# Kernel optimization log

Measured on AMD Instinct MI355X. Metric: run time of the kernel, lower is better.

Reference implementation:

```python
import jax, jax.numpy as jnp
import numpy as np

B, T, E, H = 4, 2048, 1024, 16
S = E // H

def setup_inputs() -> dict:
    key = jax.random.key(0)
    ks = jax.random.split(key, 4)
    x = jax.random.normal(ks[0], (B, T, E), dtype=jnp.float32)
    Wk = jax.random.normal(ks[1], (E, E), dtype=jnp.float32) * (E ** -0.5)
    Wq = jax.random.normal(ks[2], (E, E), dtype=jnp.float32) * (E ** -0.5)
    Wo = jax.random.normal(ks[3], (E, E), dtype=jnp.float32) * (E ** -0.5)
    bo = jnp.zeros((E,), dtype=jnp.float32)
    return {"x": x, "Wk": Wk, "Wq": Wq, "Wo": Wo, "bo": bo}

def reference(x, Wk, Wq, Wo, bo):
    b, t, e = x.shape
    h, s = H, E // H
    scale = e ** (-0.25)  # original scales q and k each by e**(1/4)
    k = (x @ Wk).reshape(b, t, h, s).transpose(0, 2, 1, 3)  # bhts
    q = (x @ Wq).reshape(b, t, h, s).transpose(0, 2, 1, 3)
    # FAITHFUL to source: values use the KEYS projection (bug in original)
    v = (x @ Wk).reshape(b, t, h, s).transpose(0, 2, 1, 3)
    dot = jnp.einsum('bhqd,bhkd->bhqk', q * scale, k * scale)
    attn = jax.nn.softmax(dot, axis=-1)
    out = jnp.einsum('bhqk,bhkd->bhqd', attn, v)
    out = out.transpose(0, 2, 1, 3).reshape(b, t, e)
    return out @ Wo + bo
```

## Files before the change

### kernel.cpp

```cpp
#include <hip/hip_runtime.h>
#include <hip/hip_bf16.h>
#include <stdint.h>

static constexpr int kB = 4;
static constexpr int kT = 2048;
static constexpr int kE = 1024;
static constexpr int kH = 16;
static constexpr int kS = 64;
static constexpr int kRows = kB * kT;

typedef __attribute__((ext_vector_type(4)))  float    f32x4;
typedef __attribute__((ext_vector_type(16))) float    f32x16;
typedef __attribute__((ext_vector_type(4)))  float    float4v;
typedef __attribute__((ext_vector_type(8)))  __bf16   bf16x8;
typedef __attribute__((ext_vector_type(8)))  short    short8v;
typedef __attribute__((ext_vector_type(4)))  short    short4v;
typedef __attribute__((ext_vector_type(2)))  unsigned u32x2;
typedef __attribute__((ext_vector_type(4)))  unsigned u32x4;

typedef const __attribute__((address_space(1))) void gvoid_t;
typedef __attribute__((address_space(3))) void lvoid_t;

__device__ __forceinline__ short f2bf(float f) {
  union { float f; unsigned u; } c; c.f = f;
  unsigned r = (c.u + 0x7FFFu + ((c.u >> 16) & 1u)) >> 16;
  return (short)(r & 0xFFFFu);
}

__device__ __forceinline__ short bfc(float f) {
  union { __bf16 b; short s; } u; u.b = (__bf16)f; return u.s;
}

__device__ __forceinline__ unsigned cvt_pk(float lo, float hi) {
  unsigned r;
  asm("v_cvt_pk_bf16_f32 %0, %1, %2" : "=v"(r) : "v"(lo), "v"(hi));
  return r;
}

__device__ __forceinline__ void plane_swap(unsigned& a, unsigned& b) {
  asm("v_permlane32_swap_b32 %0, %1" : "+v"(a), "+v"(b));
}

#if __has_builtin(__builtin_amdgcn_exp2f)
__device__ __forceinline__ float fexp2(float x) { return __builtin_amdgcn_exp2f(x); }
#else
__device__ __forceinline__ float fexp2(float x) { return exp2f(x); }
#endif

__global__ __launch_bounds__(256)
void prep(const float* __restrict__ x, const float* __restrict__ Wk,
          const float* __restrict__ Wq, const float* __restrict__ Wo,
          short* __restrict__ Xb, short* __restrict__ WkqT,
          short* __restrict__ WoT) {
  const int bid = blockIdx.x;
  if (bid < 8192) {
    size_t i = ((size_t)bid * 256 + threadIdx.x) * 4;
    float4v v = *(const float4v*)(x + i);
    short4v o;
    o[0] = f2bf(v[0]); o[1] = f2bf(v[1]); o[2] = f2bf(v[2]); o[3] = f2bf(v[3]);
    *(short4v*)(Xb + i) = o;
    return;
  }
  __shared__ float tile[32][33];
  const int tb = bid - 8192;
  const int which = tb >> 10, t = tb & 1023;
  const float* W = (which == 0) ? Wk : ((which == 1) ? Wq : Wo);
  short* WT = (which == 0) ? WkqT : ((which == 1) ? (WkqT + kE * kE) : WoT);
  const int tx = threadIdx.x & 31, ty = threadIdx.x >> 5;
  const int c = (t & 31) * 32, r = (t >> 5) * 32;
  #pragma unroll
  for (int i = ty; i < 32; i += 8)
    tile[i][tx] = W[(size_t)(r + i) * kE + c + tx];
  __syncthreads();
  #pragma unroll
  for (int i = ty; i < 32; i += 8)
    WT[(size_t)(c + i) * kE + r + tx] = f2bf(tile[tx][i]);
}

__global__ __launch_bounds__(256)
void gemm_kq(const short* __restrict__ A, const short* __restrict__ BT,
             short* __restrict__ Kb, short* __restrict__ Qb,
             short* __restrict__ KT, float qs) {
  __shared__ short SMp[16384];
  short* As = SMp;
  short* Bs = SMp + 8192;
  const int tid = threadIdx.x;
  const int w = tid >> 6, lane = tid & 63;
  const int g = lane >> 4, lr = lane & 15;
  const int bid = blockIdx.x;
  const int id = (bid & 7) * 128 + (bid >> 3);
  const int n0 = (id & 15) * 128, m0 = (id >> 4) * 128;
  const int wr = w >> 1, wc = w & 1;
  const int srow = lane >> 3, sch = lane & 7;
  const int swz = lr & 7;

  f32x4 acc[4][4];
  #pragma unroll
  for (int m = 0; m < 4; ++m)
    #pragma unroll
    for (int n = 0; n < 4; ++n)
      #pragma unroll
      for (int r = 0; r < 4; ++r) acc[m][n][r] = 0.f;

  for (int kt = 0; kt < kE; kt += 64) {
    #pragma unroll
    for (int i = 0; i < 4; ++i) {
      const int slot = w * 4 + i;
      const int row = slot * 8 + srow;
      const int sc = sch ^ srow;
      __builtin_amdgcn_global_load_lds(
          (gvoid_t*)(A + (size_t)(m0 + row) * kE + kt + 8 * sc),
          (lvoid_t*)(As + slot * 512), 16, 0, 0);
      __builtin_amdgcn_global_load_lds(
          (gvoid_t*)(BT + (size_t)(n0 + row) * kE + kt + 8 * sc),
          (lvoid_t*)(Bs + slot * 512), 16, 0, 0);
    }
    __syncthreads();
    #pragma unroll
    for (int kk = 0; kk < 2; ++kk) {
      bf16x8 af[4], bfr[4];
      #pragma unroll
      for (int m = 0; m < 4; ++m)
        af[m] = *(const bf16x8*)(As + (wr * 64 + m * 16 + lr) * 64 + (((4 * kk + g) ^ swz) << 3));
      #pragma unroll
      for (int n = 0; n < 4; ++n)
        bfr[n] = *(const bf16x8*)(Bs + (wc * 64 + n * 16 + lr) * 64 + (((4 * kk + g) ^ swz) << 3));
      __builtin_amdgcn_s_setprio(1);
      #pragma unroll
      for (int m = 0; m < 4; ++m)
        #pragma unroll
        for (int n = 0; n < 4; ++n)
          acc[m][n] = __builtin_amdgcn_mfma_f32_16x16x32_bf16(af[m], bfr[n], acc[m][n], 0, 0, 0);
      __builtin_amdgcn_s_setprio(0);
    }
    __syncthreads();
  }

  short* C = (n0 < 1024) ? Kb : Qb;
  const float scale = (n0 < 1024) ? 1.0f : qs;
  const int crow = m0 + wr * 64, ccol = (n0 & 1023) + wc * 64;
  #pragma unroll
  for (int m = 0; m < 4; ++m)
    #pragma unroll
    for (int n = 0; n < 4; ++n)
      #pragma unroll
      for (int r = 0; r < 4; ++r)
        C[(size_t)(crow + m * 16 + 4 * g + r) * kE + ccol + n * 16 + lr] =
            bfc(acc[m][n][r] * scale);

  if (n0 < 1024) {
    const int b = m0 >> 11;
    const int tloc = m0 & 2047;
    short* Lt = SMp;
    #pragma unroll
    for (int half = 0; half < 2; ++half) {
      __syncthreads();
      if (wc == half) {
        #pragma unroll
        for (int m = 0; m < 4; ++m)
          #pragma unroll
          for (int n = 0; n < 4; ++n) {
            u32x2 e;
            e[0] = cvt_pk(acc[m][n][0], acc[m][n][1]);
            e[1] = cvt_pk(acc[m][n][2], acc[m][n][3]);
            *(u32x2*)(Lt + (n * 16 + lr) * 136 + wr * 64 + m * 16 + 4 * g) = e;
          }
      }
      __syncthreads();
      const int sc = tid >> 2;
      const int h = (n0 >> 6) + half;
      short* ktrow = KT + ((size_t)(b * 16 + h) * 64 + sc) * kT + tloc;
      #pragma unroll
      for (int i = 0; i < 4; ++i) {
        const int t4 = (tid & 3) * 32 + i * 8;
        u32x4 v = *(const u32x4*)(Lt + sc * 136 + t4);
        *(u32x4*)(ktrow + t4) = v;
      }
    }
  }
}

__global__ __launch_bounds__(256)
void gemm_bt(const short* __restrict__ A, const short* __restrict__ BT,
             float* __restrict__ C, const float* __restrict__ bias,
             int M, int N, int K) {
  __shared__ short As[128 * 64];
  __shared__ short Bs[128 * 64];
  const int tid = threadIdx.x;
  const int w = tid >> 6, lane = tid & 63;
  const int g = lane >> 4, lr = lane & 15;
  const int bid = blockIdx.x;
  const int id = (bid & 7) * 64 + (bid >> 3);
  const int n0 = (id & 7) * 128, m0 = (id >> 3) * 128;
  const int wr = w >> 1, wc = w & 1;
  const int srow = lane >> 3, sch = lane & 7;
  const int swz = lr & 7;

  f32x4 acc[4][4];
  #pragma unroll
  for (int m = 0; m < 4; ++m)
    #pragma unroll
    for (int n = 0; n < 4; ++n)
      #pragma unroll
      for (int r = 0; r < 4; ++r) acc[m][n][r] = 0.f;

  for (int kt = 0; kt < K; kt += 64) {
    #pragma unroll
    for (int i = 0; i < 4; ++i) {
      const int slot = w * 4 + i;
      const int row = slot * 8 + srow;
      const int sc = sch ^ srow;
      __builtin_amdgcn_global_load_lds(
          (gvoid_t*)(A + (size_t)(m0 + row) * K + kt + 8 * sc),
          (lvoid_t*)(As + slot * 512), 16, 0, 0);
      __builtin_amdgcn_global_load_lds(
          (gvoid_t*)(BT + (size_t)(n0 + row) * K + kt + 8 * sc),
          (lvoid_t*)(Bs + slot * 512), 16, 0, 0);
    }
    __syncthreads();
    #pragma unroll
    for (int kk = 0; kk < 2; ++kk) {
      bf16x8 af[4], bfr[4];
      #pragma unroll
      for (int m = 0; m < 4; ++m)
        af[m] = *(const bf16x8*)(As + (wr * 64 + m * 16 + lr) * 64 + (((4 * kk + g) ^ swz) << 3));
      #pragma unroll
      for (int n = 0; n < 4; ++n)
        bfr[n] = *(const bf16x8*)(Bs + (wc * 64 + n * 16 + lr) * 64 + (((4 * kk + g) ^ swz) << 3));
      __builtin_amdgcn_s_setprio(1);
      #pragma unroll
      for (int m = 0; m < 4; ++m)
        #pragma unroll
        for (int n = 0; n < 4; ++n)
          acc[m][n] = __builtin_amdgcn_mfma_f32_16x16x32_bf16(af[m], bfr[n], acc[m][n], 0, 0, 0);
      __builtin_amdgcn_s_setprio(0);
    }
    __syncthreads();
  }

  const int crow = m0 + wr * 64, ccol = n0 + wc * 64;
  float bv[4];
  #pragma unroll
  for (int n = 0; n < 4; ++n) bv[n] = bias[ccol + n * 16 + lr];
  #pragma unroll
  for (int m = 0; m < 4; ++m)
    #pragma unroll
    for (int n = 0; n < 4; ++n)
      #pragma unroll
      for (int r = 0; r < 4; ++r)
        C[(size_t)(crow + m * 16 + 4 * g + r) * N + ccol + n * 16 + lr] =
            acc[m][n][r] + bv[n];
}

__global__ __launch_bounds__(256, 4)
void attn_kernel(const short* Qb, const short* __restrict__ Kb,
                 const short* __restrict__ KT, short* AO) {
  __shared__ short SM[16384];

  const int tid = threadIdx.x;
  const int w = tid >> 6, lane = tid & 63;
  const int l31 = lane & 31, hi = lane >> 5;
  const int swz = l31 & 7;
  const int bid = blockIdx.x;
  const int id = (bid & 7) * 128 + (bid >> 3);
  const int q0 = (id & 15) * 128;
  const int bh = id >> 4;
  const size_t base = (size_t)(bh >> 4) * kT * kE + (size_t)(bh & 15) * kS;
  const short* Kbh = Kb + base;
  const short* KTbh = KT + (size_t)bh * 64 * kT;

  const int srow_lo = lane >> 3, sch = lane & 7;

  #pragma unroll
  for (int i = 0; i < 2; ++i) {
    const int slot = w * 2 + i, row = slot * 8 + srow_lo;
    const int sc = sch ^ (row & 7);
    __builtin_amdgcn_global_load_lds(
        (gvoid_t*)(Kbh + (size_t)row * kE + 8 * sc),
        (lvoid_t*)(SM + slot * 512), 16, 0, 0);
    __builtin_amdgcn_global_load_lds(
        (gvoid_t*)(KTbh + (size_t)row * kT + 8 * sc),
        (lvoid_t*)(SM + 8192 + slot * 512), 16, 0, 0);
  }

  bf16x8 qB[4];
  #pragma unroll
  for (int ks = 0; ks < 4; ++ks)
    qB[ks] = *(const bf16x8*)(Qb + base +
        (size_t)(q0 + w * 32 + l31) * kE + ks * 16 + hi * 8);

  f32x16 oacc[2];
  #pragma unroll
  for (int r = 0; r < 16; ++r) { oacc[0][r] = 0.f; oacc[1][r] = 0.f; }
  float lsum = 0.f;

  for (int t = 0; t < 32; ++t) {
    __syncthreads();

    if (t < 31) {
      const short* kbt = Kbh + (size_t)(t + 1) * 64 * kE;
      const short* vtt = KTbh + (size_t)(t + 1) * 64;
      short* KtN = SM + ((t + 1) & 1) * 4096;
      short* VtN = SM + 8192 + ((t + 1) & 1) * 4096;
      #pragma unroll
      for (int i = 0; i < 2; ++i) {
        const int slot = w * 2 + i, row = slot * 8 + srow_lo;
        const int sc = sch ^ (row & 7);
        __builtin_amdgcn_global_load_lds(
            (gvoid_t*)(kbt + (size_t)row * kE + 8 * sc),
            (lvoid_t*)(KtN + slot * 512), 16, 0, 0);
        __builtin_amdgcn_global_load_lds(
            (gvoid_t*)(vtt + (size_t)row * kT + 8 * sc),
            (lvoid_t*)(VtN + slot * 512), 16, 0, 0);
      }
    }

    const short* KtC = SM + (t & 1) * 4096;
    const short* VtC = SM + 8192 + (t & 1) * 4096;

    f32x16 sacc[2];
    #pragma unroll
    for (int r = 0; r < 16; ++r) { sacc[0][r] = 0.f; sacc[1][r] = 0.f; }
    #pragma unroll
    for (int ks = 0; ks < 4; ++ks) {
      const int pc = ((2 * ks + hi) ^ swz) << 3;
      bf16x8 kf0 = *(const bf16x8*)(KtC + (l31)      * 64 + pc);
      bf16x8 kf1 = *(const bf16x8*)(KtC + (32 + l31) * 64 + pc);
      __builtin_amdgcn_s_setprio(1);
      sacc[0] = __builtin_amdgcn_mfma_f32_32x32x16_bf16(kf0, qB[ks], sacc[0], 0, 0, 0);
      sacc[1] = __builtin_amdgcn_mfma_f32_32x32x16_bf16(kf1, qB[ks], sacc[1], 0, 0, 0);
      __builtin_amdgcn_s_setprio(0);
    }

    union { unsigned u[4]; bf16x8 v; } pf[4];
    #pragma unroll
    for (int kvf = 0; kvf < 2; ++kvf) {
      float pe[16];
      #pragma unroll
      for (int r = 0; r < 16; ++r) {
        pe[r] = fexp2(sacc[kvf][r]);
        lsum += pe[r];
      }
      #pragma unroll
      for (int sub = 0; sub < 2; ++sub) {
        unsigned a0 = cvt_pk(pe[8 * sub + 0], pe[8 * sub + 1]);
        unsigned b0 = cvt_pk(pe[8 * sub + 4], pe[8 * sub + 5]);
        plane_swap(a0, b0);
        unsigned a1 = cvt_pk(pe[8 * sub + 2], pe[8 * sub + 3]);
        unsigned b1 = cvt_pk(pe[8 * sub + 6], pe[8 * sub + 7]);
        plane_swap(a1, b1);
        pf[2 * kvf + sub].u[0] = a0;
        pf[2 * kvf + sub].u[1] = a1;
        pf[2 * kvf + sub].u[2] = b0;
        pf[2 * kvf + sub].u[3] = b1;
      }
    }

    #pragma unroll
    for (int ks = 0; ks < 4; ++ks) {
      const int pc = ((2 * ks + hi) ^ swz) << 3;
      bf16x8 vf0 = *(const bf16x8*)(VtC + (l31)      * 64 + pc);
      bf16x8 vf1 = *(const bf16x8*)(VtC + (32 + l31) * 64 + pc);
      __builtin_amdgcn_s_setprio(1);
      oacc[0] = __builtin_amdgcn_mfma_f32_32x32x16_bf16(vf0, pf[ks].v, oacc[0], 0, 0, 0);
      oacc[1] = __builtin_amdgcn_mfma_f32_32x32x16_bf16(vf1, pf[ks].v, oacc[1], 0, 0, 0);
      __builtin_amdgcn_s_setprio(0);
    }
  }

  __syncthreads();

  const float ltot = lsum + __shfl_xor(lsum, 32);
  const float inv = 1.f / ltot;
  short* OtW = SM + w * 2176;
  #pragma unroll
  for (int sf = 0; sf < 2; ++sf)
    #pragma unroll
    for (int c = 0; c < 4; ++c) {
      u32x2 e;
      e[0] = cvt_pk(oacc[sf][4 * c + 0] * inv, oacc[sf][4 * c + 1] * inv);
      e[1] = cvt_pk(oacc[sf][4 * c + 2] * inv, oacc[sf][4 * c + 3] * inv);
      *(u32x2*)(OtW + l31 * 68 + sf * 32 + 8 * c + 4 * hi) = e;
    }
  __builtin_amdgcn_s_barrier();
  #pragma unroll
  for (int i = 0; i < 8; ++i) {
    const int row = i * 4 + (lane >> 4);
    u32x2 v = *(const u32x2*)(OtW + row * 68 + (lane & 15) * 4);
    *(u32x2*)(AO + base + (size_t)(q0 + w * 32 + row) * kE + (lane & 15) * 4) = v;
  }
}

extern "C" void kernel_launch(void* const* d_in, const int* in_sizes, int n_in,
                              void* d_out, int out_size, void* d_ws, size_t ws_size,
                              hipStream_t stream) {
  const float* x  = (const float*)d_in[0];
  const float* Wk = (const float*)d_in[1];
  const float* Wq = (const float*)d_in[2];
  const float* Wo = (const float*)d_in[3];
  const float* bo = (const float*)d_in[4];
  float* out = (float*)d_out;

  const size_t nXE = (size_t)kRows * kE;
  const size_t nW  = (size_t)kE * kE;

  short* Xb   = (short*)d_ws;
  short* Kb   = Xb   + nXE;
  short* Qb   = Kb   + nXE;
  short* WkqT = Qb   + nXE;
  short* WoT  = WkqT + 2 * nW;
  short* KTb  = (short*)d_out;
  short* AO   = Qb;

  prep<<<dim3(8192 + 3 * 1024), 256, 0, stream>>>(
      x, Wk, Wq, Wo, Xb, WkqT, WoT);

  gemm_kq<<<dim3(1024), 256, 0, stream>>>(
      Xb, WkqT, Kb, Qb, KTb, 0.03125f * 1.44269504f);

  attn_kernel<<<dim3(1024), 256, 0, stream>>>(Qb, Kb, KTb, AO);

  gemm_bt<<<dim3(512), 256, 0, stream>>>(
      AO, WoT, out, bo, kRows, kE, kE);
}
```

Baseline: 172.5 us.

## Rewrite K/Q projection GEMM as 256x256 double-buffered 8-wave pipelined kernel

Replaces the 128x128, 4-wave K/Q projection GEMM with a 256x256 tile kernel using 8 waves. It double-buffers LDS and interleaves global-to-LDS loads of the next K-slab with MFMA phases, using explicit barriers, waitcnt and priority hints. The larger tile raises reuse per loaded byte, and the overlap is meant to hide load latency. The transposed K write now goes straight from registers to global memory instead of through an LDS staging pass, which may give less coalesced stores. The kernel uses 128KB of LDS and many accumulator registers, which limits occupancy to one block per CU.

```diff
diff --git a/kernel.cpp b/kernel.cpp
--- a/kernel.cpp
+++ b/kernel.cpp
@@ -77,106 +77,192 @@
     WT[(size_t)(c + i) * kE + r + tx] = f2bf(tile[tx][i]);
 }
 
-__global__ __launch_bounds__(256)
-void gemm_kq(const short* __restrict__ A, const short* __restrict__ BT,
-             short* __restrict__ Kb, short* __restrict__ Qb,
-             short* __restrict__ KT, float qs) {
-  __shared__ short SMp[16384];
-  short* As = SMp;
-  short* Bs = SMp + 8192;
+
+__device__ __forceinline__ void kq_stageA(
+    const short* __restrict__ gA, short* nA, int wid, int sl, int sc7) {
+  #pragma unroll
+  for (int h = 0; h < 2; ++h)
+    #pragma unroll
+    for (int i = 0; i < 2; ++i) {
+      const int slot = wid * 2 + i;
+      const int row = slot * 8 + sl;
+      const int sc = sc7 ^ (row & 7);
+      __builtin_amdgcn_global_load_lds(
+          (gvoid_t*)(gA + (size_t)(h * 128 + row) * kE + 8 * sc),
+          (lvoid_t*)(nA + h * 8192 + slot * 512), 16, 0, 0);
+    }
+}
+
+__device__ __forceinline__ void kq_tile(
+    const short* __restrict__ gA, const short* __restrict__ gB,
+    const short* cA, const short* cB, short* nA, short* nB,
+    bool stage, f32x4 (&acc)[8][4],
+    int wid, int wm, int wn, int g, int lr, int sl, int sc7) {
+  const int swz = lr & 7;
+  const short* cAw = cA + wm * 8192;
+  const short* cBw = cB + (wn >> 1) * 8192;
+  const int brow0 = (wn & 1) * 64;
+  bf16x8 af[4][2], b0[2][2], b1[2][2];
+
+  #pragma unroll
+  for (int mf = 0; mf < 4; ++mf)
+    #pragma unroll
+    for (int kk = 0; kk < 2; ++kk)
+      af[mf][kk] = *(const bf16x8*)(cAw + (mf * 16 + lr) * 64 + (((4 * kk + g) ^ swz) << 3));
+  #pragma unroll
+  for (int nf = 0; nf < 2; ++nf)
+    #pragma unroll
+    for (int kk = 0; kk < 2; ++kk)
+      b0[nf][kk] = *(const bf16x8*)(cBw + (brow0 + nf * 16 + lr) * 64 + (((4 * kk + g) ^ swz) << 3));
+  if (stage) kq_stageA(gA, nA, wid, sl, sc7);
+  asm volatile("" ::: "memory");
+  __builtin_amdgcn_s_barrier();
+  asm volatile("s_waitcnt lgkmcnt(0)" ::: "memory");
+  __builtin_amdgcn_sched_barrier(0);
+  __builtin_amdgcn_s_setprio(1);
+  #pragma unroll
+  for (int mf = 0; mf < 4; ++mf)
+    #pragma unroll
+    for (int nf = 0; nf < 2; ++nf)
+      #pragma unroll
+      for (int kk = 0; kk < 2; ++kk)
+        acc[mf][nf] = __builtin_amdgcn_mfma_f32_16x16x32_bf16(af[mf][kk], b0[nf][kk], acc[mf][nf], 0, 0, 0);
+  __builtin_amdgcn_s_setprio(0);
+  asm volatile("" ::: "memory");
+  __builtin_amdgcn_s_barrier();
+
+  #pragma unroll
+  for (int nf = 0; nf < 2; ++nf)
+    #pragma unroll
+    for (int kk = 0; kk < 2; ++kk)
+      b1[nf][kk] = *(const bf16x8*)(cBw + (brow0 + 32 + nf * 16 + lr) * 64 + (((4 * kk + g) ^ swz) << 3));
+  if (stage) kq_stageA(gB, nB, wid, sl, sc7);
+  asm volatile("" ::: "memory");
+  __builtin_amdgcn_s_barrier();
+  asm volatile("s_waitcnt lgkmcnt(0)" ::: "memory");
+  __builtin_amdgcn_sched_barrier(0);
+  __builtin_amdgcn_s_setprio(1);
+  #pragma unroll
+  for (int mf = 0; mf < 4; ++mf)
+    #pragma unroll
+    for (int nf = 0; nf < 2; ++nf)
+      #pragma unroll
+      for (int kk = 0; kk < 2; ++kk)
+        acc[mf][2 + nf] = __builtin_amdgcn_mfma_f32_16x16x32_bf16(af[mf][kk], b1[nf][kk], acc[mf][2 + nf], 0, 0, 0);
+  __builtin_amdgcn_s_setprio(0);
+  asm volatile("" ::: "memory");
+  __builtin_amdgcn_s_barrier();
+
+  #pragma unroll
+  for (int mf = 0; mf < 4; ++mf)
+    #pragma unroll
+    for (int kk = 0; kk < 2; ++kk)
+      af[mf][kk] = *(const bf16x8*)(cAw + (64 + mf * 16 + lr) * 64 + (((4 * kk + g) ^ swz) << 3));
+  asm volatile("" ::: "memory");
+  __builtin_amdgcn_s_barrier();
+  asm volatile("s_waitcnt lgkmcnt(0)" ::: "memory");
+  __builtin_amdgcn_sched_barrier(0);
+  __builtin_amdgcn_s_setprio(1);
+  #pragma unroll
+  for (int mf = 0; mf < 4; ++mf)
+    #pragma unroll
+    for (int nf = 0; nf < 2; ++nf)
+      #pragma unroll
+      for (int kk = 0; kk < 2; ++kk)
+        acc[4 + mf][2 + nf] = __builtin_amdgcn_mfma_f32_16x16x32_bf16(af[mf][kk], b1[nf][kk], acc[4 + mf][2 + nf], 0, 0, 0);
+  __builtin_amdgcn_s_setprio(0);
+  asm volatile("" ::: "memory");
+  __builtin_amdgcn_s_barrier();
+
+  #pragma unroll
+  for (int nf = 0; nf < 2; ++nf)
+    #pragma unroll
+    for (int kk = 0; kk < 2; ++kk)
+      b0[nf][kk] = *(const bf16x8*)(cBw + (brow0 + nf * 16 + lr) * 64 + (((4 * kk + g) ^ swz) << 3));
+  asm volatile("s_waitcnt vmcnt(0)" ::: "memory");
+  asm volatile("" ::: "memory");
+  __builtin_amdgcn_s_barrier();
+  asm volatile("s_waitcnt lgkmcnt(0)" ::: "memory");
+  __builtin_amdgcn_sched_barrier(0);
+  __builtin_amdgcn_s_setprio(1);
+  #pragma unroll
+  for (int mf = 0; mf < 4; ++mf)
+    #pragma unroll
+    for (int nf = 0; nf < 2; ++nf)
+      #pragma unroll
+      for (int kk = 0; kk < 2; ++kk)
+        acc[4 + mf][nf] = __builtin_amdgcn_mfma_f32_16x16x32_bf16(af[mf][kk], b0[nf][kk], acc[4 + mf][nf], 0, 0, 0);
+  __builtin_amdgcn_s_setprio(0);
+  asm volatile("" ::: "memory");
+  __builtin_amdgcn_s_barrier();
+}
+
+__global__ __launch_bounds__(512)
+void gemm_kq8(const short* __restrict__ A, const short* __restrict__ BT,
+              short* __restrict__ Kb, short* __restrict__ Qb,
+              short* __restrict__ KT, float qs) {
+  __shared__ short LA[2][16384];
+  __shared__ short LB[2][16384];
+
   const int tid = threadIdx.x;
-  const int w = tid >> 6, lane = tid & 63;
+  const int wid = tid >> 6, lane = tid & 63;
   const int g = lane >> 4, lr = lane & 15;
+  const int wm = wid >> 2, wn = wid & 3;
+  const int sl = lane >> 3, sc7 = lane & 7;
   const int bid = blockIdx.x;
-  const int id = (bid & 7) * 128 + (bid >> 3);
-  const int n0 = (id & 15) * 128, m0 = (id >> 4) * 128;
-  const int wr = w >> 1, wc = w & 1;
-  const int srow = lane >> 3, sch = lane & 7;
-  const int swz = lr & 7;
-
-  f32x4 acc[4][4];
-  #pragma unroll
-  for (int m = 0; m < 4; ++m)
-    #pragma unroll
-    for (int n = 0; n < 4; ++n)
-      #pragma unroll
-      for (int r = 0; r < 4; ++r) acc[m][n][r] = 0.f;
-
-  for (int kt = 0; kt < kE; kt += 64) {
-    #pragma unroll
-    for (int i = 0; i < 4; ++i) {
-      const int slot = w * 4 + i;
-      const int row = slot * 8 + srow;
-      const int sc = sch ^ srow;
-      __builtin_amdgcn_global_load_lds(
-          (gvoid_t*)(A + (size_t)(m0 + row) * kE + kt + 8 * sc),
-          (lvoid_t*)(As + slot * 512), 16, 0, 0);
-      __builtin_amdgcn_global_load_lds(
-          (gvoid_t*)(BT + (size_t)(n0 + row) * kE + kt + 8 * sc),
-          (lvoid_t*)(Bs + slot * 512), 16, 0, 0);
-    }
-    __syncthreads();
-    #pragma unroll
-    for (int kk = 0; kk < 2; ++kk) {
-      bf16x8 af[4], bfr[4];
-      #pragma unroll
-      for (int m = 0; m < 4; ++m)
-        af[m] = *(const bf16x8*)(As + (wr * 64 + m * 16 + lr) * 64 + (((4 * kk + g) ^ swz) << 3));
-      #pragma unroll
-      for (int n = 0; n < 4; ++n)
-        bfr[n] = *(const bf16x8*)(Bs + (wc * 64 + n * 16 + lr) * 64 + (((4 * kk + g) ^ swz) << 3));
-      __builtin_amdgcn_s_setprio(1);
-      #pragma unroll
-      for (int m = 0; m < 4; ++m)
-        #pragma unroll
-        for (int n = 0; n < 4; ++n)
-          acc[m][n] = __builtin_amdgcn_mfma_f32_16x16x32_bf16(af[m], bfr[n], acc[m][n], 0, 0, 0);
-      __builtin_amdgcn_s_setprio(0);
-    }
-    __syncthreads();
-  }
-
-  short* C = (n0 < 1024) ? Kb : Qb;
-  const float scale = (n0 < 1024) ? 1.0f : qs;
-  const int crow = m0 + wr * 64, ccol = (n0 & 1023) + wc * 64;
-  #pragma unroll
-  for (int m = 0; m < 4; ++m)
-    #pragma unroll
-    for (int n = 0; n < 4; ++n)
+  const int id = (bid & 7) * 32 + (bid >> 3);
+  const int n0 = (id & 7) * 256, m0 = (id >> 3) * 256;
+
+  const short* Abase = A + (size_t)m0 * kE;
+  const short* Bbase = BT + (size_t)n0 * kE;
+
+  f32x4 acc[8][4];
+  #pragma unroll
+  for (int mf = 0; mf < 8; ++mf)
+    #pragma unroll
+    for (int nf = 0; nf < 4; ++nf)
+      #pragma unroll
+      for (int r = 0; r < 4; ++r) acc[mf][nf][r] = 0.f;
+
+  kq_stageA(Abase, &LA[0][0], wid, sl, sc7);
+  kq_stageA(Bbase, &LB[0][0], wid, sl, sc7);
+  asm volatile("s_waitcnt vmcnt(0)" ::: "memory");
+  __syncthreads();
+
+  for (int ktp = 0; ktp < 8; ++ktp) {
+    kq_tile(Abase + (2 * ktp + 1) * 64, Bbase + (2 * ktp + 1) * 64,
+            &LA[0][0], &LB[0][0], &LA[1][0], &LB[1][0],
+            true, acc, wid, wm, wn, g, lr, sl, sc7);
+    kq_tile(Abase + (2 * ktp + 2) * 64, Bbase + (2 * ktp + 2) * 64,
+            &LA[1][0], &LB[1][0], &LA[0][0], &LB[0][0],
+            (2 * ktp + 1) < 15, acc, wid, wm, wn, g, lr, sl, sc7);
+  }
+
+  const int isq = (n0 >= 1024);
+  short* Crm = isq ? Qb : Kb;
+  const float scale = isq ? qs : 1.0f;
+  const int crow = m0 + wm * 128, ccol = (n0 & 1023) + wn * 64;
+  #pragma unroll
+  for (int mf = 0; mf < 8; ++mf)
+    #pragma unroll
+    for (int nf = 0; nf < 4; ++nf)
       #pragma unroll
       for (int r = 0; r < 4; ++r)
-        C[(size_t)(crow + m * 16 + 4 * g + r) * kE + ccol + n * 16 + lr] =
-            bfc(acc[m][n][r] * scale);
-
-  if (n0 < 1024) {
-    const int b = m0 >> 11;
-    const int tloc = m0 & 2047;
-    short* Lt = SMp;
-    #pragma unroll
-    for (int half = 0; half < 2; ++half) {
-      __syncthreads();
-      if (wc == half) {
-        #pragma unroll
-        for (int m = 0; m < 4; ++m)
-          #pragma unroll
-          for (int n = 0; n < 4; ++n) {
-            u32x2 e;
-            e[0] = cvt_pk(acc[m][n][0], acc[m][n][1]);
-            e[1] = cvt_pk(acc[m][n][2], acc[m][n][3]);
-            *(u32x2*)(Lt + (n * 16 + lr) * 136 + wr * 64 + m * 16 + 4 * g) = e;
-          }
+        Crm[(size_t)(crow + mf * 16 + 4 * g + r) * kE + ccol + nf * 16 + lr] =
+            bfc(acc[mf][nf][r] * scale);
+  if (!isq) {
+    const int b = m0 >> 11, tloc = (m0 & 2047) + wm * 128;
+    const int h = (n0 + wn * 64) >> 6;
+    #pragma unroll
+    for (int mf = 0; mf < 8; ++mf)
+      #pragma unroll
+      for (int nf = 0; nf < 4; ++nf) {
+        u32x2 e;
+        e[0] = cvt_pk(acc[mf][nf][0], acc[mf][nf][1]);
+        e[1] = cvt_pk(acc[mf][nf][2], acc[mf][nf][3]);
+        *(u32x2*)(KT + (size_t)((b * 16 + h) * 64 + nf * 16 + lr) * kT +
+                  tloc + mf * 16 + 4 * g) = e;
       }
-      __syncthreads();
-      const int sc = tid >> 2;
-      const int h = (n0 >> 6) + half;
-      short* ktrow = KT + ((size_t)(b * 16 + h) * 64 + sc) * kT + tloc;
-      #pragma unroll
-      for (int i = 0; i < 4; ++i) {
-        const int t4 = (tid & 3) * 32 + i * 8;
-        u32x4 v = *(const u32x4*)(Lt + sc * 136 + t4);
-        *(u32x4*)(ktrow + t4) = v;
-      }
-    }
   }
 }
 
@@ -415,7 +501,7 @@
   prep<<<dim3(8192 + 3 * 1024), 256, 0, stream>>>(
       x, Wk, Wq, Wo, Xb, WkqT, WoT);
 
-  gemm_kq<<<dim3(1024), 256, 0, stream>>>(
+  gemm_kq8<<<dim3(256), 512, 0, stream>>>(
       Xb, WkqT, Kb, Qb, KTb, 0.03125f * 1.44269504f);
 
   attn_kernel<<<dim3(1024), 256, 0, stream>>>(Qb, Kb, KTb, AO);
```

New measurement: 162.0 us. 6.1% less time.
